# Kernel tuning notes

Hardware: AMD Instinct MI355X
Metric: run time of the kernel (lower is better)

The kernel has to match this reference:

```python
import jax, jax.numpy as jnp
import numpy as np

N_ENT = 100000
N_REL = 12
D = 64
E = 1000000
LAYER_DIMS = [64, 32]


def _xavier(key, shape):
    fan_in, fan_out = shape[-1], shape[-2] if len(shape) >= 2 else shape[-1]
    std = np.sqrt(2.0 / (fan_in + fan_out)).astype(np.float32)
    return jax.random.normal(key, shape, jnp.float32) * std


def setup_inputs() -> dict:
    key = jax.random.key(0)
    ks = jax.random.split(key, 14)
    return {
        "entity_emb": _xavier(ks[0], (N_ENT, D)),
        "rel_emb": _xavier(ks[1], (N_REL, D)),
        "W_r": _xavier(ks[2], (N_REL, D, D)),
        "W1_0_w": _xavier(ks[3], (LAYER_DIMS[0], D)),
        "W1_0_b": jnp.zeros((LAYER_DIMS[0],), jnp.float32),
        "W2_0_w": _xavier(ks[4], (LAYER_DIMS[0], D)),
        "W2_0_b": jnp.zeros((LAYER_DIMS[0],), jnp.float32),
        "W1_1_w": _xavier(ks[5], (LAYER_DIMS[1], LAYER_DIMS[0])),
        "W1_1_b": jnp.zeros((LAYER_DIMS[1],), jnp.float32),
        "W2_1_w": _xavier(ks[6], (LAYER_DIMS[1], LAYER_DIMS[0])),
        "W2_1_b": jnp.zeros((LAYER_DIMS[1],), jnp.float32),
        "src": jax.random.randint(ks[7], (E,), 0, N_ENT, jnp.int32),
        "dst": jax.random.randint(ks[8], (E,), 0, N_ENT, jnp.int32),
        "etype": jax.random.randint(ks[9], (E,), 0, N_REL, jnp.int32),
    }


def reference(entity_emb, rel_emb, W_r, W1_0_w, W1_0_b, W2_0_w, W2_0_b,
              W1_1_w, W1_1_b, W2_1_w, W2_1_b, src, dst, etype):
    n = entity_emb.shape[0]

    # --- compute_attention: per-edge TransR scores, edge_softmax over dst ---
    # Instead of gathering W_r[etype] per edge ([E,D,D] is huge), project every
    # node by every relation matrix once: [N, R, Dr].
    proj = jnp.einsum('nd,kdr->nkr', entity_emb, W_r)
    tail = proj[src, etype]          # [E, Dr] (src projected by its edge's W_r)
    head = proj[dst, etype]          # [E, Dr]
    rel = rel_emb[etype]             # [E, Dr]
    logits = jnp.sum(tail * jnp.tanh(head + rel), axis=-1)  # [E]

    # edge softmax grouped by destination node (stable)
    m = jax.ops.segment_max(logits, dst, num_segments=n)
    ex = jnp.exp(logits - m[dst])
    den = jax.ops.segment_sum(ex, dst, num_segments=n)
    att = ex / den[dst]              # [E]

    # --- KGATLayer: gather-scale-scatter + bi-interaction (dropout = 0) ---
    def layer(x, W1w, W1b, W2w, W2b):
        h_n = jax.ops.segment_sum(x[src] * att[:, None], dst, num_segments=n)
        add = jax.nn.leaky_relu((x + h_n) @ W1w.T + W1b)
        mul = jax.nn.leaky_relu((x * h_n) @ W2w.T + W2b)
        return add + mul

    x0 = entity_emb
    x1 = layer(x0, W1_0_w, W1_0_b, W2_0_w, W2_0_b)
    x2 = layer(x1, W1_1_w, W1_1_b, W2_1_w, W2_1_b)
    # embedder concatenates the input and every layer output
    return jnp.concatenate([x0, x1, x2], axis=1)  # [N, 64+64+32]
```

## Files before the change

### kernel.cpp

```cpp
#include <hip/hip_runtime.h>
#include <hip/hip_bf16.h>
#include <math.h>


typedef __attribute__((ext_vector_type(8))) short short8;
typedef __attribute__((ext_vector_type(4))) float float4v;

__device__ __forceinline__ short f2bf(float f) {
  __hip_bfloat16 h = __float2bfloat16(f);
  return *(short*)&h;
}
__device__ __forceinline__ float bf2f(short s) {
  return __uint_as_float(((unsigned)(unsigned short)s) << 16);
}

#define LOG2E 1.4426950408889634f

__global__ void k_prep(const float* __restrict__ emb, short* __restrict__ emb_h,
                       const float* __restrict__ Wr, short* __restrict__ Bt,
                       const float* __restrict__ W10, const float* __restrict__ W20,
                       const float* __restrict__ W11, const float* __restrict__ W21,
                       short* __restrict__ w1h0, short* __restrict__ w1l0,
                       short* __restrict__ w2h0, short* __restrict__ w2l0,
                       short* __restrict__ w1h1, short* __restrict__ w1l1,
                       short* __restrict__ w2h1, short* __restrict__ w2l1,
                       const int* __restrict__ src, const int* __restrict__ dst,
                       const int* __restrict__ et, int* __restrict__ bcur,
                       uint2* __restrict__ stg, int nE, int bsh, int cap,
                       int nb1, int nb_cvt, int n4) {
  __shared__ int hist[256];
  __shared__ int base[256];
  int b = blockIdx.x, t = threadIdx.x;
  if (b < nb1) {
    hist[t] = 0;
    __syncthreads();
    int tile = b * 8192;
#pragma unroll 4
    for (int j = 0; j < 32; j++) {
      int e = tile + j * 256 + t;
      if (e < nE) atomicAdd(&hist[dst[e] >> bsh], 1);
    }
    __syncthreads();
    int cnt = hist[t];
    if (cnt > 0) base[t] = atomicAdd(&bcur[t], cnt);
    hist[t] = 0;
    __syncthreads();
#pragma unroll 4
    for (int j = 0; j < 32; j++) {
      int e = tile + j * 256 + t;
      if (e < nE) {
        int d = dst[e], bk = d >> bsh;
        int r = atomicAdd(&hist[bk], 1);
        stg[(size_t)bk * cap + base[bk] + r] =
            make_uint2((unsigned)src[e], (unsigned)d | ((unsigned)et[e] << 20));
      }
    }
    return;
  }
  int b2 = b - nb1;
  if (b2 < nb_cvt) {
    int i = b2 * 256 + t;
    if (i < n4) {
      float4 v = ((const float4*)emb)[i];
      union { short s[4]; uint2 u; } o;
      o.s[0] = f2bf(v.x); o.s[1] = f2bf(v.y); o.s[2] = f2bf(v.z); o.s[3] = f2bf(v.w);
      ((uint2*)emb_h)[i] = o.u;
    }
  } else if (b2 < nb_cvt + 12) {
    int k = b2 - nb_cvt;
    for (int i = t; i < 4096; i += 256) {
      int d = i >> 6, r = i & 63;
      Bt[k * 4096 + r * 64 + d] = f2bf(Wr[k * 4096 + i]);
    }
  } else {
    int i = (b2 - nb_cvt - 12) * 256 + t;
    const float* W; short* H; short* L; int j;
    if (i < 4096) { W = W10; H = w1h0; L = w1l0; j = i; }
    else if (i < 8192) { W = W20; H = w2h0; L = w2l0; j = i - 4096; }
    else if (i < 10240) { W = W11; H = w1h1; L = w1l1; j = i - 8192; }
    else if (i < 12288) { W = W21; H = w2h1; L = w2l1; j = i - 10240; }
    else return;
    float w = W[j];
    short hi = f2bf(w);
    H[j] = hi;
    L[j] = f2bf(w - bf2f(hi));
  }
}

__global__ __launch_bounds__(256) void k_projm(const short* __restrict__ A,
                                               const short* __restrict__ Bt,
                                               short* __restrict__ proj,
                                               int n_ent) {
  __shared__ unsigned short sh[4][32 * 72];
  int wave = threadIdx.x >> 6, lane = threadIdx.x & 63;
  int quad = lane >> 4, l16 = lane & 15;
  int m0 = blockIdx.x * 128 + wave * 32;
  unsigned short* W = &sh[wave][0];
  short8 a[2][2];
#pragma unroll
  for (int mt = 0; mt < 2; mt++)
#pragma unroll
    for (int kc = 0; kc < 2; kc++) {
      int row = m0 + mt * 16 + l16;
      int rr = row < n_ent ? row : 0;
      a[mt][kc] = *(const short8*)(A + (size_t)rr * 64 + kc * 32 + quad * 8);
    }
  for (int k = 0; k < 12; k++) {
    const short* B = Bt + k * 4096;
    short8 b[4][2];
#pragma unroll
    for (int nt = 0; nt < 4; nt++)
#pragma unroll
      for (int kc = 0; kc < 2; kc++)
        b[nt][kc] = *(const short8*)(B + (nt * 16 + l16) * 64 + kc * 32 + quad * 8);
    float4v acc[2][4];
#pragma unroll
    for (int mt = 0; mt < 2; mt++)
#pragma unroll
      for (int nt = 0; nt < 4; nt++)
        acc[mt][nt] = (float4v){0.f, 0.f, 0.f, 0.f};
#pragma unroll
    for (int kc = 0; kc < 2; kc++)
#pragma unroll
      for (int mt = 0; mt < 2; mt++)
#pragma unroll
        for (int nt = 0; nt < 4; nt++)
          acc[mt][nt] = __builtin_amdgcn_mfma_f32_16x16x32_bf16(
              a[mt][kc], b[nt][kc], acc[mt][nt], 0, 0, 0);
#pragma unroll
    for (int mt = 0; mt < 2; mt++)
#pragma unroll
      for (int nt = 0; nt < 4; nt++)
#pragma unroll
        for (int r = 0; r < 4; r++) {
          int row = mt * 16 + quad * 4 + r;
          int col = nt * 16 + l16;
          W[row * 72 + col] = (unsigned short)f2bf(acc[mt][nt][r]);
        }
    const size_t plane = (size_t)k * n_ent;
#pragma unroll
    for (int i = 0; i < 4; i++) {
      int row = (lane >> 3) + 8 * i;
      int cs = (lane & 7) * 8;
      short8 v = *(const short8*)(W + row * 72 + cs);
      int node = m0 + row;
      if (node < n_ent)
        *(short8*)(proj + (plane + node) * 64 + cs) = v;
    }
  }
}

__global__ void k_bscan(const int* __restrict__ bcur, int* __restrict__ bbase,
                        int* __restrict__ row_ptr, int nbuck, int n, int nE) {
  __shared__ int s[256];
  int t = threadIdx.x;
  int v = (t < nbuck) ? bcur[t] : 0;
  s[t] = v;
  __syncthreads();
  for (int o = 1; o < 256; o <<= 1) {
    int a = (t >= o) ? s[t - o] : 0;
    __syncthreads();
    s[t] += a;
    __syncthreads();
  }
  if (t < nbuck) bbase[t] = s[t] - v;
  if (t == 0) row_ptr[n] = nE;
}

__global__ __launch_bounds__(256) void k_bsort2(const uint2* __restrict__ stg,
                                                const int* __restrict__ bcur,
                                                const int* __restrict__ bbase,
                                                int* __restrict__ row_ptr,
                                                uint2* __restrict__ csr2,
                                                int n, int bsh, int cap) {
  __shared__ int cnt[1024];
  __shared__ int sc[1024];
  int b = blockIdx.x, t = threadIdx.x;
  int lo = b << bsh;
  if (lo > n) lo = n;
  int hi = (b + 1) << bsh;
  if (hi > n) hi = n;
  int w = hi - lo;
#pragma unroll
  for (int j = 0; j < 4; j++) cnt[t + j * 256] = 0;
  __syncthreads();
  int m = bcur[b];
  const uint2* S = stg + (size_t)b * cap;
  for (int p = t; p < m; p += 256)
    atomicAdd(&cnt[(int)(S[p].y & 0xFFFFFu) - lo], 1);
  __syncthreads();
#pragma unroll
  for (int j = 0; j < 4; j++) sc[t + j * 256] = cnt[t + j * 256];
  __syncthreads();
  for (int o = 1; o < 1024; o <<= 1) {
    int a[4];
#pragma unroll
    for (int j = 0; j < 4; j++) {
      int i = t + j * 256;
      a[j] = (i >= o) ? sc[i - o] : 0;
    }
    __syncthreads();
#pragma unroll
    for (int j = 0; j < 4; j++) sc[t + j * 256] += a[j];
    __syncthreads();
  }
  int gbase = bbase[b];
#pragma unroll
  for (int j = 0; j < 4; j++) {
    int i = t + j * 256;
    if (i < w) {
      int c0 = gbase + sc[i] - cnt[i];
      row_ptr[lo + i] = c0;
      cnt[i] = c0;
    }
  }
  __syncthreads();
  for (int p = t; p < m; p += 256) {
    uint2 v = S[p];
    int d = (int)(v.y & 0xFFFFFu);
    int pos = atomicAdd(&cnt[d - lo], 1);
    csr2[pos] = v;
  }
}

__global__ __launch_bounds__(256) void k_logits(const short* __restrict__ ps,
                                                const float* __restrict__ rel_emb,
                                                uint2* csr2, int nE, int n_ent) {
  int t = threadIdx.x;
  int lane = t & 63;
  int sub = lane >> 3;
  int c8 = (lane & 7) * 8;
  int e0 = (blockIdx.x * 4 + (t >> 6)) * 32;
  if (e0 >= nE) return;
  int ku[4];
  short8 tl[4], hd[4];
#pragma unroll
  for (int u = 0; u < 4; u++) {
    int e = e0 + u * 8 + sub;
    int ee = e < nE ? e : nE - 1;
    uint2 c = csr2[ee];
    int s = (int)c.x;
    int d = (int)(c.y & 0xFFFFFu);
    int k = (int)(c.y >> 20);
    ku[u] = k;
    const size_t plane = (size_t)k * n_ent;
    tl[u] = *(const short8*)(ps + (plane + s) * 64 + c8);
    hd[u] = *(const short8*)(ps + (plane + d) * 64 + c8);
  }
  float v[4];
#pragma unroll
  for (int u = 0; u < 4; u++) {
    const float* rp = rel_emb + ku[u] * 64 + c8;
    float4 r0 = *(const float4*)rp;
    float4 r1 = *(const float4*)(rp + 4);
    float rr[8] = {r0.x, r0.y, r0.z, r0.w, r1.x, r1.y, r1.z, r1.w};
    float vv = 0.f;
#pragma unroll
    for (int q = 0; q < 8; q++) {
      float x = bf2f(hd[u][q]) + rr[q];
      float tt = __builtin_amdgcn_exp2f(x * (2.f * LOG2E));
      float r = __builtin_amdgcn_rcpf(tt + 1.f);
      float th = fmaf(-2.f, r, 1.f);
      vv = fmaf(bf2f(tl[u][q]), th, vv);
    }
    vv += __shfl_xor(vv, 1);
    vv += __shfl_xor(vv, 2);
    vv += __shfl_xor(vv, 4);
    v[u] = __builtin_amdgcn_exp2f(vv * LOG2E);
  }
  int uu = lane & 7;
  if (uu < 4) {
    float myv = v[0];
    if (uu == 1) myv = v[1];
    if (uu == 2) myv = v[2];
    if (uu == 3) myv = v[3];
    int e = e0 + uu * 8 + sub;
    if (e < nE) csr2[e].y = __float_as_uint(myv);
  }
}

__global__ __launch_bounds__(256) void k_agg(const short* __restrict__ xh,
                                             const int* __restrict__ row_ptr,
                                             const uint2* __restrict__ csr,
                                             float* __restrict__ hn, int n_ent) {
  int wave = threadIdx.x >> 6, lane = threadIdx.x & 63;
  int n = blockIdx.x * 4 + wave;
  if (n >= n_ent) return;
  int jb = row_ptr[n], je = row_ptr[n + 1];
  int deg = je - jb;
  if (deg == 0) {
    hn[(size_t)n * 64 + lane] = 0.f;
    return;
  }
  uint2 c = (lane < deg) ? csr[jb + lane] : make_uint2(0u, 0u);
  int sidx = (int)c.x;
  float exv = (lane < deg) ? __uint_as_float(c.y) : 0.f;
  float den = exv;
#pragma unroll
  for (int o = 32; o; o >>= 1) den += __shfl_xor(den, o);
  int m = deg < 64 ? deg : 64;
  float acc = 0.f;
  for (int j = 0; j < m; j += 8) {
    int s0 = __shfl(sidx, j), s1 = __shfl(sidx, j + 1);
    int s2 = __shfl(sidx, j + 2), s3 = __shfl(sidx, j + 3);
    int s4 = __shfl(sidx, j + 4), s5 = __shfl(sidx, j + 5);
    int s6 = __shfl(sidx, j + 6), s7 = __shfl(sidx, j + 7);
    float e0 = __shfl(exv, j), e1 = __shfl(exv, j + 1);
    float e2 = __shfl(exv, j + 2), e3 = __shfl(exv, j + 3);
    float e4 = __shfl(exv, j + 4), e5 = __shfl(exv, j + 5);
    float e6 = __shfl(exv, j + 6), e7 = __shfl(exv, j + 7);
    short g0 = xh[(size_t)s0 * 64 + lane];
    short g1 = xh[(size_t)s1 * 64 + lane];
    short g2 = xh[(size_t)s2 * 64 + lane];
    short g3 = xh[(size_t)s3 * 64 + lane];
    short g4 = xh[(size_t)s4 * 64 + lane];
    short g5 = xh[(size_t)s5 * 64 + lane];
    short g6 = xh[(size_t)s6 * 64 + lane];
    short g7 = xh[(size_t)s7 * 64 + lane];
    acc = fmaf(e0, bf2f(g0), acc); acc = fmaf(e1, bf2f(g1), acc);
    acc = fmaf(e2, bf2f(g2), acc); acc = fmaf(e3, bf2f(g3), acc);
    acc = fmaf(e4, bf2f(g4), acc); acc = fmaf(e5, bf2f(g5), acc);
    acc = fmaf(e6, bf2f(g6), acc); acc = fmaf(e7, bf2f(g7), acc);
  }
  if (deg > 64) {
    for (int jj = jb + 64; jj < je; jj++) {
      uint2 cc = csr[jj];
      float ee = __uint_as_float(cc.y);
      den += ee;
      acc = fmaf(ee, bf2f(xh[(size_t)cc.x * 64 + lane]), acc);
    }
  }
  hn[(size_t)n * 64 + lane] = acc / den;
}

template <int OD, bool FIRST>
__global__ __launch_bounds__(256) void k_upmfma(const float* __restrict__ x,
                                                const float* __restrict__ hn,
                                                const short* __restrict__ g1h,
                                                const short* __restrict__ g1l,
                                                const short* __restrict__ g2h,
                                                const short* __restrict__ g2l,
                                                const float* __restrict__ b1,
                                                const float* __restrict__ b2,
                                                float* __restrict__ out,
                                                float* __restrict__ x_next,
                                                short* __restrict__ xh_next,
                                                int n_ent) {
  constexpr int NT = OD / 16;
  __shared__ short w1h[OD * 72], w1l[OD * 72], w2h[OD * 72], w2l[OD * 72];
  int t = threadIdx.x;
  for (int i = t; i < OD * 16; i += 256) {
    int o = i >> 4, dq = (i & 15) * 4;
    *(uint2*)(w1h + o * 72 + dq) = *(const uint2*)(g1h + o * 64 + dq);
    *(uint2*)(w1l + o * 72 + dq) = *(const uint2*)(g1l + o * 64 + dq);
    *(uint2*)(w2h + o * 72 + dq) = *(const uint2*)(g2h + o * 64 + dq);
    *(uint2*)(w2l + o * 72 + dq) = *(const uint2*)(g2l + o * 64 + dq);
  }
  int wave = t >> 6, lane = t & 63;
  int quad = lane >> 4, l16 = lane & 15;
  int m0 = blockIdx.x * 128 + wave * 32;
  float4v accA[2][NT], accM[2][NT];
#pragma unroll
  for (int mt = 0; mt < 2; mt++)
#pragma unroll
    for (int nt = 0; nt < NT; nt++) {
      accA[mt][nt] = (float4v){0.f, 0.f, 0.f, 0.f};
      accM[mt][nt] = (float4v){0.f, 0.f, 0.f, 0.f};
    }
  __syncthreads();
#pragma unroll
  for (int kc = 0; kc < 2; kc++) {
    short8 ah_add[2], al_add[2], ah_mul[2], al_mul[2];
#pragma unroll
    for (int mt = 0; mt < 2; mt++) {
      int row = m0 + mt * 16 + l16;
      int rr = row < n_ent ? row : 0;
      const float* xp = x + (size_t)rr * 64 + kc * 32 + quad * 8;
      const float* hp = hn + (size_t)rr * 64 + kc * 32 + quad * 8;
      float4 xa = *(const float4*)xp;
      float4 xb = *(const float4*)(xp + 4);
      float4 ha = *(const float4*)hp;
      float4 hb = *(const float4*)(hp + 4);
      if (FIRST && row < n_ent) {
        *(float4*)(out + (size_t)row * 160 + kc * 32 + quad * 8) = xa;
        *(float4*)(out + (size_t)row * 160 + kc * 32 + quad * 8 + 4) = xb;
      }
      float xs[8] = {xa.x, xa.y, xa.z, xa.w, xb.x, xb.y, xb.z, xb.w};
      float hs[8] = {ha.x, ha.y, ha.z, ha.w, hb.x, hb.y, hb.z, hb.w};
#pragma unroll
      for (int q = 0; q < 8; q++) {
        float s = xs[q] + hs[q];
        short shi = f2bf(s);
        ah_add[mt][q] = shi;
        al_add[mt][q] = f2bf(s - bf2f(shi));
        float p = xs[q] * hs[q];
        short phi = f2bf(p);
        ah_mul[mt][q] = phi;
        al_mul[mt][q] = f2bf(p - bf2f(phi));
      }
    }
#pragma unroll
    for (int nt = 0; nt < NT; nt++) {
      int boff = (nt * 16 + l16) * 72 + kc * 32 + quad * 8;
      short8 b1h = *(const short8*)(w1h + boff);
      short8 b1l = *(const short8*)(w1l + boff);
      short8 b2h = *(const short8*)(w2h + boff);
      short8 b2l = *(const short8*)(w2l + boff);
#pragma unroll
      for (int mt = 0; mt < 2; mt++) {
        accA[mt][nt] = __builtin_amdgcn_mfma_f32_16x16x32_bf16(
            ah_add[mt], b1h, accA[mt][nt], 0, 0, 0);
        accA[mt][nt] = __builtin_amdgcn_mfma_f32_16x16x32_bf16(
            al_add[mt], b1h, accA[mt][nt], 0, 0, 0);
        accA[mt][nt] = __builtin_amdgcn_mfma_f32_16x16x32_bf16(
            ah_add[mt], b1l, accA[mt][nt], 0, 0, 0);
        accM[mt][nt] = __builtin_amdgcn_mfma_f32_16x16x32_bf16(
            ah_mul[mt], b2h, accM[mt][nt], 0, 0, 0);
        accM[mt][nt] = __builtin_amdgcn_mfma_f32_16x16x32_bf16(
            al_mul[mt], b2h, accM[mt][nt], 0, 0, 0);
        accM[mt][nt] = __builtin_amdgcn_mfma_f32_16x16x32_bf16(
            ah_mul[mt], b2l, accM[mt][nt], 0, 0, 0);
      }
    }
  }
#pragma unroll
  for (int nt = 0; nt < NT; nt++) {
    int col = nt * 16 + l16;
    float bb1 = b1[col], bb2 = b2[col];
#pragma unroll
    for (int mt = 0; mt < 2; mt++) {
#pragma unroll
      for (int r = 0; r < 4; r++) {
        int row = m0 + mt * 16 + quad * 4 + r;
        float aa = accA[mt][nt][r] + bb1;
        float mm = accM[mt][nt][r] + bb2;
        aa = aa > 0.f ? aa : 0.01f * aa;
        mm = mm > 0.f ? mm : 0.01f * mm;
        float y = aa + mm;
        if constexpr (FIRST) {
          float yn = __shfl_xor(y, 1);
          if (row < n_ent) {
            out[(size_t)row * 160 + 64 + col] = y;
            x_next[(size_t)row * 64 + col] = y;
            if ((lane & 1) == 0) {
              unsigned pk = (unsigned)(unsigned short)f2bf(y) |
                            ((unsigned)(unsigned short)f2bf(yn) << 16);
              *(unsigned*)(xh_next + (size_t)row * 64 + col) = pk;
            }
          }
        } else {
          if (row < n_ent) out[(size_t)row * 160 + 128 + col] = y;
        }
      }
    }
  }
}

extern "C" void kernel_launch(void* const* d_in, const int* in_sizes, int n_in,
                              void* d_out, int out_size, void* d_ws, size_t ws_size,
                              hipStream_t stream) {
  const float* emb = (const float*)d_in[0];
  const float* rel = (const float*)d_in[1];
  const float* Wr = (const float*)d_in[2];
  const float* W10w = (const float*)d_in[3];
  const float* W10b = (const float*)d_in[4];
  const float* W20w = (const float*)d_in[5];
  const float* W20b = (const float*)d_in[6];
  const float* W11w = (const float*)d_in[7];
  const float* W11b = (const float*)d_in[8];
  const float* W21w = (const float*)d_in[9];
  const float* W21b = (const float*)d_in[10];
  const int* src = (const int*)d_in[11];
  const int* dst = (const int*)d_in[12];
  const int* et = (const int*)d_in[13];
  int N = in_sizes[0] / 64;
  int E = in_sizes[11];
  float* out = (float*)d_out;

  int bsh = 9;
  while (((N + (1 << bsh) - 1) >> bsh) > 256) bsh++;
  int nbuck = (N + (1 << bsh) - 1) >> bsh;
  int cap = ((E / nbuck) * 3 / 2 + 1024 + 255) / 256 * 256;

  char* p = (char*)d_ws;
  auto alloc = [&](size_t bytes) -> char* {
    char* r = p;
    p += (bytes + 255) / 256 * 256;
    return r;
  };
  short* proj = (short*)alloc((size_t)N * 768 * 2);
  uint2* csr2 = (uint2*)alloc((size_t)E * 8);
  uint2* stg = (uint2*)alloc((size_t)nbuck * cap * 8);
  int* row_ptr = (int*)alloc((size_t)(N + 1) * 4);
  int* bcur = (int*)alloc(1024);
  int* bbase = (int*)alloc(2048);
  float* hn = (float*)alloc((size_t)N * 64 * 4);
  float* x1 = (float*)alloc((size_t)N * 64 * 4);
  short* emb_h = (short*)alloc(((size_t)N + 128) * 64 * 2);
  short* x1h = (short*)alloc(((size_t)N + 128) * 64 * 2);
  short* Bt = (short*)alloc((size_t)12 * 4096 * 2);
  short* w1h0 = (short*)alloc(4096 * 2);
  short* w1l0 = (short*)alloc(4096 * 2);
  short* w2h0 = (short*)alloc(4096 * 2);
  short* w2l0 = (short*)alloc(4096 * 2);
  short* w1h1 = (short*)alloc(2048 * 2);
  short* w1l1 = (short*)alloc(2048 * 2);
  short* w2h1 = (short*)alloc(2048 * 2);
  short* w2l1 = (short*)alloc(2048 * 2);

  int n4 = N * 16;
  int nb_cvt = (n4 + 255) / 256;
  int nb1 = (E + 8191) / 8192;

  hipMemsetAsync(bcur, 0, 1024, stream);
  k_prep<<<nb1 + nb_cvt + 60, 256, 0, stream>>>(
      emb, emb_h, Wr, Bt, W10w, W20w, W11w, W21w,
      w1h0, w1l0, w2h0, w2l0, w1h1, w1l1, w2h1, w2l1,
      src, dst, et, bcur, stg, E, bsh, cap, nb1, nb_cvt, n4);
  k_projm<<<(N + 127) / 128, 256, 0, stream>>>(emb_h, Bt, proj, N);
  k_bscan<<<1, 256, 0, stream>>>(bcur, bbase, row_ptr, nbuck, N, E);
  k_bsort2<<<nbuck, 256, 0, stream>>>(stg, bcur, bbase, row_ptr, csr2, N, bsh, cap);
  k_logits<<<(E + 127) / 128, 256, 0, stream>>>(proj, rel, csr2, E, N);
  k_agg<<<(N + 3) / 4, 256, 0, stream>>>(emb_h, row_ptr, csr2, hn, N);
  k_upmfma<64, true><<<(N + 127) / 128, 256, 0, stream>>>(
      emb, hn, w1h0, w1l0, w2h0, w2l0, W10b, W20b, out, x1, x1h, N);
  k_agg<<<(N + 3) / 4, 256, 0, stream>>>(x1h, row_ptr, csr2, hn, N);
  k_upmfma<32, false><<<(N + 127) / 128, 256, 0, stream>>>(
      x1, hn, w1h1, w1l1, w2h1, w2l1, W11b, W21b, out, nullptr, nullptr, N);
}
```

Baseline: 406.9 us.

## Shrink bucketing and projection tiles, fold bucket scan into sort kernel

The edge-bucketing stage in the prep kernel now uses 2048-edge tiles instead of 8192, giving four times as many blocks, with a fully unrolled loop. The projection GEMM kernel handles 16 rows per wave instead of 32, so it launches twice as many blocks with fewer registers each. The separate single-block bucket scan kernel is removed: every sort block recomputes the 256-entry prefix scan itself, saving one launch at the cost of redundant scan work. More tiles also means more global atomics on the bucket counters, and each projection block reloads the B matrices for fewer rows.

Result: slower. 416.5 us (+2.4%).

```diff
diff --git a/kernel.cpp b/kernel.cpp
--- a/kernel.cpp
+++ b/kernel.cpp
@@ -15,6 +15,7 @@
 }
 
 #define LOG2E 1.4426950408889634f
+#define BS1_TILE 2048
 
 __global__ void k_prep(const float* __restrict__ emb, short* __restrict__ emb_h,
                        const float* __restrict__ Wr, short* __restrict__ Bt,
@@ -34,9 +35,9 @@
   if (b < nb1) {
     hist[t] = 0;
     __syncthreads();
-    int tile = b * 8192;
-#pragma unroll 4
-    for (int j = 0; j < 32; j++) {
+    int tile = b * BS1_TILE;
+#pragma unroll
+    for (int j = 0; j < BS1_TILE / 256; j++) {
       int e = tile + j * 256 + t;
       if (e < nE) atomicAdd(&hist[dst[e] >> bsh], 1);
     }
@@ -45,8 +46,8 @@
     if (cnt > 0) base[t] = atomicAdd(&bcur[t], cnt);
     hist[t] = 0;
     __syncthreads();
-#pragma unroll 4
-    for (int j = 0; j < 32; j++) {
+#pragma unroll
+    for (int j = 0; j < BS1_TILE / 256; j++) {
       int e = tile + j * 256 + t;
       if (e < nE) {
         int d = dst[e], bk = d >> bsh;
@@ -91,20 +92,18 @@
                                                const short* __restrict__ Bt,
                                                short* __restrict__ proj,
                                                int n_ent) {
-  __shared__ unsigned short sh[4][32 * 72];
+  __shared__ unsigned short sh[4][16 * 72];
   int wave = threadIdx.x >> 6, lane = threadIdx.x & 63;
   int quad = lane >> 4, l16 = lane & 15;
-  int m0 = blockIdx.x * 128 + wave * 32;
+  int m0 = blockIdx.x * 64 + wave * 16;
   unsigned short* W = &sh[wave][0];
-  short8 a[2][2];
-#pragma unroll
-  for (int mt = 0; mt < 2; mt++)
-#pragma unroll
-    for (int kc = 0; kc < 2; kc++) {
-      int row = m0 + mt * 16 + l16;
-      int rr = row < n_ent ? row : 0;
-      a[mt][kc] = *(const short8*)(A + (size_t)rr * 64 + kc * 32 + quad * 8);
-    }
+  short8 a[2];
+#pragma unroll
+  for (int kc = 0; kc < 2; kc++) {
+    int row = m0 + l16;
+    int rr = row < n_ent ? row : 0;
+    a[kc] = *(const short8*)(A + (size_t)rr * 64 + kc * 32 + quad * 8);
+  }
   for (int k = 0; k < 12; k++) {
     const short* B = Bt + k * 4096;
     short8 b[4][2];
@@ -113,33 +112,23 @@
 #pragma unroll
       for (int kc = 0; kc < 2; kc++)
         b[nt][kc] = *(const short8*)(B + (nt * 16 + l16) * 64 + kc * 32 + quad * 8);
-    float4v acc[2][4];
-#pragma unroll
-    for (int mt = 0; mt < 2; mt++)
+    float4v acc[4];
+#pragma unroll
+    for (int nt = 0; nt < 4; nt++) acc[nt] = (float4v){0.f, 0.f, 0.f, 0.f};
+#pragma unroll
+    for (int kc = 0; kc < 2; kc++)
 #pragma unroll
       for (int nt = 0; nt < 4; nt++)
-        acc[mt][nt] = (float4v){0.f, 0.f, 0.f, 0.f};
-#pragma unroll
-    for (int kc = 0; kc < 2; kc++)
-#pragma unroll
-      for (int mt = 0; mt < 2; mt++)
-#pragma unroll
-        for (int nt = 0; nt < 4; nt++)
-          acc[mt][nt] = __builtin_amdgcn_mfma_f32_16x16x32_bf16(
-              a[mt][kc], b[nt][kc], acc[mt][nt], 0, 0, 0);
-#pragma unroll
-    for (int mt = 0; mt < 2; mt++)
-#pragma unroll
-      for (int nt = 0; nt < 4; nt++)
-#pragma unroll
-        for (int r = 0; r < 4; r++) {
-          int row = mt * 16 + quad * 4 + r;
-          int col = nt * 16 + l16;
-          W[row * 72 + col] = (unsigned short)f2bf(acc[mt][nt][r]);
-        }
+        acc[nt] = __builtin_amdgcn_mfma_f32_16x16x32_bf16(
+            a[kc], b[nt][kc], acc[nt], 0, 0, 0);
+#pragma unroll
+    for (int nt = 0; nt < 4; nt++)
+#pragma unroll
+      for (int r = 0; r < 4; r++)
+        W[(quad * 4 + r) * 72 + nt * 16 + l16] = (unsigned short)f2bf(acc[nt][r]);
     const size_t plane = (size_t)k * n_ent;
 #pragma unroll
-    for (int i = 0; i < 4; i++) {
+    for (int i = 0; i < 2; i++) {
       int row = (lane >> 3) + 8 * i;
       int cs = (lane & 7) * 8;
       short8 v = *(const short8*)(W + row * 72 + cs);
@@ -150,32 +139,26 @@
   }
 }
 
-__global__ void k_bscan(const int* __restrict__ bcur, int* __restrict__ bbase,
-                        int* __restrict__ row_ptr, int nbuck, int n, int nE) {
-  __shared__ int s[256];
-  int t = threadIdx.x;
+__global__ __launch_bounds__(256) void k_bsort2(const uint2* __restrict__ stg,
+                                                const int* __restrict__ bcur,
+                                                int* __restrict__ row_ptr,
+                                                uint2* __restrict__ csr2,
+                                                int n, int bsh, int cap,
+                                                int nbuck, int nE) {
+  __shared__ int cnt[1024];
+  __shared__ int sc[1024];
+  __shared__ int bs[256];
+  int b = blockIdx.x, t = threadIdx.x;
   int v = (t < nbuck) ? bcur[t] : 0;
-  s[t] = v;
+  bs[t] = v;
   __syncthreads();
   for (int o = 1; o < 256; o <<= 1) {
-    int a = (t >= o) ? s[t - o] : 0;
-    __syncthreads();
-    s[t] += a;
-    __syncthreads();
-  }
-  if (t < nbuck) bbase[t] = s[t] - v;
-  if (t == 0) row_ptr[n] = nE;
-}
-
-__global__ __launch_bounds__(256) void k_bsort2(const uint2* __restrict__ stg,
-                                                const int* __restrict__ bcur,
-                                                const int* __restrict__ bbase,
-                                                int* __restrict__ row_ptr,
-                                                uint2* __restrict__ csr2,
-                                                int n, int bsh, int cap) {
-  __shared__ int cnt[1024];
-  __shared__ int sc[1024];
-  int b = blockIdx.x, t = threadIdx.x;
+    int a = (t >= o) ? bs[t - o] : 0;
+    __syncthreads();
+    bs[t] += a;
+    __syncthreads();
+  }
+  int gbase = bs[b] - bcur[b];
   int lo = b << bsh;
   if (lo > n) lo = n;
   int hi = (b + 1) << bsh;
@@ -204,7 +187,6 @@
     for (int j = 0; j < 4; j++) sc[t + j * 256] += a[j];
     __syncthreads();
   }
-  int gbase = bbase[b];
 #pragma unroll
   for (int j = 0; j < 4; j++) {
     int i = t + j * 256;
@@ -214,12 +196,13 @@
       cnt[i] = c0;
     }
   }
+  if (b == nbuck - 1 && t == 0) row_ptr[n] = nE;
   __syncthreads();
   for (int p = t; p < m; p += 256) {
-    uint2 v = S[p];
-    int d = (int)(v.y & 0xFFFFFu);
+    uint2 vv = S[p];
+    int d = (int)(vv.y & 0xFFFFFu);
     int pos = atomicAdd(&cnt[d - lo], 1);
-    csr2[pos] = v;
+    csr2[pos] = vv;
   }
 }
 
@@ -493,7 +476,6 @@
   uint2* stg = (uint2*)alloc((size_t)nbuck * cap * 8);
   int* row_ptr = (int*)alloc((size_t)(N + 1) * 4);
   int* bcur = (int*)alloc(1024);
-  int* bbase = (int*)alloc(2048);
   float* hn = (float*)alloc((size_t)N * 64 * 4);
   float* x1 = (float*)alloc((size_t)N * 64 * 4);
   short* emb_h = (short*)alloc(((size_t)N + 128) * 64 * 2);
@@ -510,16 +492,15 @@
 
   int n4 = N * 16;
   int nb_cvt = (n4 + 255) / 256;
-  int nb1 = (E + 8191) / 8192;
+  int nb1 = (E + BS1_TILE - 1) / BS1_TILE;
 
   hipMemsetAsync(bcur, 0, 1024, stream);
   k_prep<<<nb1 + nb_cvt + 60, 256, 0, stream>>>(
       emb, emb_h, Wr, Bt, W10w, W20w, W11w, W21w,
       w1h0, w1l0, w2h0, w2l0, w1h1, w1l1, w2h1, w2l1,
       src, dst, et, bcur, stg, E, bsh, cap, nb1, nb_cvt, n4);
-  k_projm<<<(N + 127) / 128, 256, 0, stream>>>(emb_h, Bt, proj, N);
-  k_bscan<<<1, 256, 0, stream>>>(bcur, bbase, row_ptr, nbuck, N, E);
-  k_bsort2<<<nbuck, 256, 0, stream>>>(stg, bcur, bbase, row_ptr, csr2, N, bsh, cap);
+  k_projm<<<(N + 63) / 64, 256, 0, stream>>>(emb_h, Bt, proj, N);
+  k_bsort2<<<nbuck, 256, 0, stream>>>(stg, bcur, row_ptr, csr2, N, bsh, cap, nbuck, E);
   k_logits<<<(E + 127) / 128, 256, 0, stream>>>(proj, rel, csr2, E, N);
   k_agg<<<(N + 3) / 4, 256, 0, stream>>>(emb_h, row_ptr, csr2, hn, N);
   k_upmfma<64, true><<<(N + 127) / 128, 256, 0, stream>>>(
```
